# Kernel tuning notes

Measured on AMD Instinct MI355X. Metric: run time of the kernel, lower is better.

The kernel has to match this reference:

```python
import jax, jax.numpy as jnp
import numpy as np

H = 256; NH = 4; DH = H // NH
NT, NS, NV = 4096, 2048, 1024
E1, E2, E3 = 65536, 16384, 32768
LN_EPS = 1e-5


def setup_inputs() -> dict:
    key = jax.random.key(0)
    ks = jax.random.split(key, 40)
    def nrm(i, shape):
        return jax.random.normal(ks[i], shape, jnp.float32) * 0.05
    inp = {
        "x_term": jax.random.normal(ks[0], (NT, H), jnp.float32),
        "x_symbol": jax.random.normal(ks[1], (NS, H), jnp.float32),
        "x_var": jax.random.normal(ks[2], (NV, H), jnp.float32),
        "ha_src": jax.random.randint(ks[3], (E1,), 0, NT),
        "ha_dst": jax.random.randint(ks[4], (E1,), 0, NT),
        "so_src": jax.random.randint(ks[5], (E2,), 0, NT),
        "so_dst": jax.random.randint(ks[6], (E2,), 0, NS),
        "vo_src": jax.random.randint(ks[7], (E3,), 0, NV),
        "vo_dst": jax.random.randint(ks[8], (E3,), 0, NT),
        # SAGEConv params for the 4 term-destination relations
        "Wl_rha": nrm(9, (H, H)),  "bl_rha": nrm(10, (H,)), "Wr_rha": nrm(11, (H, H)),
        "Wl_ha":  nrm(12, (H, H)), "bl_ha":  nrm(13, (H,)), "Wr_ha":  nrm(14, (H, H)),
        "Wl_rsym": nrm(15, (H, H)), "bl_rsym": nrm(16, (H,)), "Wr_rsym": nrm(17, (H, H)),
        "Wl_var": nrm(18, (H, H)), "bl_var": nrm(19, (H,)), "Wr_var": nrm(20, (H, H)),
        "ln_g": jnp.ones((H,), jnp.float32),
        "ln_b": jnp.zeros((H,), jnp.float32),
        "in_proj_w": nrm(21, (3 * H, H)),
        "in_proj_b": nrm(22, (3 * H,)),
        "out_proj_w": nrm(23, (H, H)),
        "out_proj_b": nrm(24, (H,)),
        "post_w": nrm(25, (H, H)),
        "post_b": nrm(26, (H,)),
    }
    return inp


def _sage(x_src, x_dst, src, dst, Wl, bl, Wr, num_dst):
    # PyG SAGEConv: lin_l(mean_j x_src[j]) + lin_r(x_dst)
    msg = x_src[src]                                            # [E, H] gather
    s = jax.ops.segment_sum(msg, dst, num_segments=num_dst)     # [N_dst, H] scatter-add
    cnt = jax.ops.segment_sum(jnp.ones((src.shape[0],), x_src.dtype), dst,
                              num_segments=num_dst)
    agg = s / jnp.maximum(cnt, 1.0)[:, None]
    return agg @ Wl.T + bl + x_dst @ Wr.T


def _layernorm(x, g, b):
    mu = jnp.mean(x, axis=-1, keepdims=True)
    var = jnp.mean(jnp.square(x - mu), axis=-1, keepdims=True)
    return (x - mu) * jax.lax.rsqrt(var + LN_EPS) * g + b


def _mha(x, in_w, in_b, out_w, out_b):
    # torch MultiheadAttention (eval, batch=1, self-attention)
    qkv = x @ in_w.T + in_b                       # [N, 3H]
    q, k, v = jnp.split(qkv, 3, axis=-1)
    def heads(t):
        return t.reshape(-1, NH, DH).transpose(1, 0, 2)  # [NH, N, DH]
    q, k, v = heads(q), heads(k), heads(v)
    scores = jnp.einsum("hqd,hkd->hqk", q, k) / np.sqrt(DH).astype(np.float32)
    a = jax.nn.softmax(scores, axis=-1)
    o = jnp.einsum("hqk,hkd->hqd", a, v)          # [NH, N, DH]
    o = o.transpose(1, 0, 2).reshape(-1, H)
    return o @ out_w.T + out_b


def reference(x_term, x_symbol, x_var,
              ha_src, ha_dst, so_src, so_dst, vo_src, vo_dst,
              Wl_rha, bl_rha, Wr_rha, Wl_ha, bl_ha, Wr_ha,
              Wl_rsym, bl_rsym, Wr_rsym, Wl_var, bl_var, Wr_var,
              ln_g, ln_b, in_proj_w, in_proj_b, out_proj_w, out_proj_b,
              post_w, post_b):
    nt = x_term.shape[0]
    # HeteroConv(aggr='sum') over the 4 relations whose destination is 'term'
    conv_term = (
        _sage(x_term, x_term, ha_dst, ha_src, Wl_rha, bl_rha, Wr_rha, nt)    # rev_has_arg
        + _sage(x_term, x_term, ha_src, ha_dst, Wl_ha, bl_ha, Wr_ha, nt)     # has_arg
        + _sage(x_symbol, x_term, so_dst, so_src, Wl_rsym, bl_rsym, Wr_rsym, nt)  # rev_symbol_of
        + _sage(x_var, x_term, vo_src, vo_dst, Wl_var, bl_var, Wr_var, nt)   # var_occurrence
    )
    term_out = _layernorm(conv_term + x_term, ln_g, ln_b)  # dropout is identity in eval
    attn_out = _mha(term_out, in_proj_w, in_proj_b, out_proj_w, out_proj_b)
    post = jax.nn.relu(attn_out @ post_w.T + post_b)
    term_final = post + term_out
    return term_final
```

## Files before the change

### kernel.cpp

```cpp
#include <hip/hip_runtime.h>
#include <hip/hip_bf16.h>

#define H 256
#define NT 4096
#define NHEAD 4
#define E1 65536
#define E2 16384
#define E3 32768
#define TOTE (2 * E1 + E2 + E3)
#define LN_EPS 1e-5f
#define SPLIT 4

typedef __hip_bfloat16 bf16;
typedef short bf16x8 __attribute__((ext_vector_type(8)));
typedef float f32x4 __attribute__((ext_vector_type(4)));

__device__ __forceinline__ float b2f(bf16 v) { return __bfloat162float(v); }
__device__ __forceinline__ float u2f(unsigned short u) {
    unsigned int x = ((unsigned int)u) << 16;
    return __uint_as_float(x);
}
__device__ __forceinline__ unsigned short f2u(float f) {
    bf16 h = __float2bfloat16(f);
    unsigned short v;
    __builtin_memcpy(&v, &h, 2);
    return v;
}
__device__ __forceinline__ float ldin(const void* p, size_t i, bool isbf) {
    return isbf ? b2f(((const bf16*)p)[i]) : ((const float*)p)[i];
}

__global__ __launch_bounds__(256) void k_init(float4* cnt4, int n4,
                                              const unsigned int* __restrict__ lng,
                                              unsigned int* __restrict__ flag) {
    int i = blockIdx.x * 256 + threadIdx.x;
    if (i == 0) *flag = (lng[0] == 0x3F803F80u) ? 1u : 0u;
    int stride = gridDim.x * 256;
    float4 z = make_float4(0.f, 0.f, 0.f, 0.f);
    for (; i < n4; i += stride) cnt4[i] = z;
}

__global__ __launch_bounds__(256) void k_count4(const int* __restrict__ s0, const int* __restrict__ s1,
                                                const int* __restrict__ s2, const int* __restrict__ s3,
                                                int* __restrict__ cnt) {
    int i = blockIdx.x * 256 + threadIdx.x;
    int r, e;
    if (i < E1) { r = 0; e = i; }
    else if (i < 2 * E1) { r = 1; e = i - E1; }
    else if (i < 2 * E1 + E2) { r = 2; e = i - 2 * E1; }
    else if (i < TOTE) { r = 3; e = i - 2 * E1 - E2; }
    else return;
    const int* s = (r == 0) ? s0 : (r == 1) ? s1 : (r == 2) ? s2 : s3;
    atomicAdd(&cnt[r * NT + s[e]], 1);
}

__global__ __launch_bounds__(256) void k_scan(const int* __restrict__ cnt, int* __restrict__ offs,
                                              int* __restrict__ cursor) {
    __shared__ int tot[256];
    int t = threadIdx.x, r = blockIdx.x;
    const int* c = cnt + r * NT;
    int* o = offs + r * (NT + 1);
    int* cur = cursor + r * NT;
    int base = t * 16;
    int local[16];
    int sum = 0;
#pragma unroll
    for (int j = 0; j < 16; j++) { local[j] = c[base + j]; sum += local[j]; }
    tot[t] = sum;
    __syncthreads();
    if (t == 0) {
        int run = 0;
        for (int i = 0; i < 256; i++) { int v = tot[i]; tot[i] = run; run += v; }
        o[NT] = run;
    }
    __syncthreads();
    int run = tot[t];
#pragma unroll
    for (int j = 0; j < 16; j++) { o[base + j] = run; cur[base + j] = run; run += local[j]; }
}

__global__ __launch_bounds__(256) void k_fill(const int* __restrict__ s0, const int* __restrict__ s1,
                                              const int* __restrict__ s2, const int* __restrict__ s3,
                                              const int* __restrict__ g0, const int* __restrict__ g1,
                                              const int* __restrict__ g2, const int* __restrict__ g3,
                                              int* __restrict__ cursor, int* __restrict__ csr) {
    int i = blockIdx.x * 256 + threadIdx.x;
    int r, e, rb;
    if (i < E1) { r = 0; e = i; rb = 0; }
    else if (i < 2 * E1) { r = 1; e = i - E1; rb = E1; }
    else if (i < 2 * E1 + E2) { r = 2; e = i - 2 * E1; rb = 2 * E1; }
    else if (i < TOTE) { r = 3; e = i - 2 * E1 - E2; rb = 2 * E1 + E2; }
    else return;
    const int* s = (r == 0) ? s0 : (r == 1) ? s1 : (r == 2) ? s2 : s3;
    const int* g = (r == 0) ? g0 : (r == 1) ? g1 : (r == 2) ? g2 : g3;
    int d = s[e];
    int pos = atomicAdd(&cursor[r * NT + d], 1);
    csr[rb + pos] = g[e];
}

__global__ __launch_bounds__(256) void k_gatherA(
    const void* __restrict__ x0, const void* __restrict__ x1,
    const void* __restrict__ x2, const void* __restrict__ x3,
    const int* __restrict__ offs, const int* __restrict__ csr,
    bf16* __restrict__ aggs, const unsigned int* __restrict__ flag) {
    int y = blockIdx.y;
    int i = blockIdx.x * 4 + (threadIdx.x >> 6);
    int lane = threadIdx.x & 63;
    bool isbf = (*flag != 0u);
    const void* x = (y == 0) ? x0 : (y == 1) ? x1 : (y == 2) ? x2 : x3;
    static const int rbase[4] = {0, E1, 2 * E1, 2 * E1 + E2};
    const int* o = offs + y * (NT + 1);
    const int* cs = csr + rbase[y];
    int b = o[i], e = o[i + 1];
    float ax = 0.f, ay = 0.f, az = 0.f, aw = 0.f;
    if (isbf) {
        for (int j = b; j < e; j++) {
            int s = cs[j];
            ushort4 u = *(const ushort4*)((const unsigned short*)x + (size_t)s * H + lane * 4);
            ax += u2f(u.x); ay += u2f(u.y); az += u2f(u.z); aw += u2f(u.w);
        }
    } else {
        for (int j = b; j < e; j++) {
            int s = cs[j];
            float4 v = *(const float4*)((const float*)x + (size_t)s * H + lane * 4);
            ax += v.x; ay += v.y; az += v.z; aw += v.w;
        }
    }
    float inv = 1.0f / fmaxf((float)(e - b), 1.0f);
    *(ushort4*)((unsigned short*)aggs + ((size_t)y * NT + i) * H + lane * 4) =
        make_ushort4(f2u(ax * inv), f2u(ay * inv), f2u(az * inv), f2u(aw * inv));
}

__global__ __launch_bounds__(256) void k_prepB(
    const void* __restrict__ Wl0, const void* __restrict__ Wl1,
    const void* __restrict__ Wl2, const void* __restrict__ Wl3,
    const void* __restrict__ Wr0, const void* __restrict__ Wr1,
    const void* __restrict__ Wr2, const void* __restrict__ Wr3,
    const void* __restrict__ b0, const void* __restrict__ b1,
    const void* __restrict__ b2, const void* __restrict__ b3,
    bf16* __restrict__ Bcat, float* __restrict__ bsum, const unsigned int* __restrict__ flag) {
    int idx = blockIdx.x * 256 + threadIdx.x;
    bool isbf = (*flag != 0u);
    int n = idx / 1280, k = idx % 1280;
    float v;
    if (k < 1024) {
        const void* W = (k < 256) ? Wl0 : (k < 512) ? Wl1 : (k < 768) ? Wl2 : Wl3;
        v = ldin(W, (size_t)n * 256 + (k & 255), isbf);
    } else {
        size_t o = (size_t)n * 256 + (k - 1024);
        v = ldin(Wr0, o, isbf) + ldin(Wr1, o, isbf) + ldin(Wr2, o, isbf) + ldin(Wr3, o, isbf);
    }
    ((unsigned short*)Bcat)[idx] = f2u(v);
    if (idx < 256)
        bsum[idx] = ldin(b0, idx, isbf) + ldin(b1, idx, isbf) + ldin(b2, idx, isbf) + ldin(b3, idx, isbf);
}

__global__ __launch_bounds__(256) void k_convln(
    const bf16* __restrict__ aggs, const bf16* __restrict__ Bcat, const float* __restrict__ bsum,
    const void* __restrict__ xt, const void* __restrict__ gw, const void* __restrict__ gb,
    bf16* __restrict__ term, const unsigned int* __restrict__ flag) {
    __shared__ unsigned short Asm[8 * 16 * 8];
    __shared__ unsigned short Bsm[8 * 256 * 8];
    __shared__ float redS[4][16];
    const bool isbf = (*flag != 0u);
    const int tid = threadIdx.x;
    const int w = tid >> 6, lane = tid & 63;
    const int col = lane & 15, quad = lane >> 4;
    const int m0 = blockIdx.x * 16;
    const int srow = tid & 63, skq = tid >> 6;

    f32x4 acc[4];
#pragma unroll
    for (int dt = 0; dt < 4; dt++) acc[dt] = (f32x4){0.f, 0.f, 0.f, 0.f};

    bf16x8 areg;
    bf16x8 breg[8];
    auto loadA = [&](int k0) {
        if (tid < 128) {
            int row = tid & 15, akq = tid >> 4;
            int k = k0 + akq * 8;
            if (k < 1024) {
                areg = *(const bf16x8*)((const unsigned short*)aggs +
                                        ((size_t)(k >> 8) * NT + m0 + row) * 256 + (k & 255));
            } else {
#pragma unroll
                for (int j = 0; j < 8; j++)
                    areg[j] = (short)f2u(ldin(xt, (size_t)(m0 + row) * 256 + (k - 1024) + j, isbf));
            }
        }
    };
    auto loadB = [&](int k0) {
#pragma unroll
        for (int t = 0; t < 4; t++)
#pragma unroll
            for (int kk = 0; kk < 2; kk++)
                breg[t * 2 + kk] = *(const bf16x8*)((const unsigned short*)Bcat +
                                       (size_t)(t * 64 + srow) * 1280 + k0 + (skq * 2 + kk) * 8);
    };

    loadA(0);
    loadB(0);
    for (int k0 = 0; k0 < 1280; k0 += 64) {
        __syncthreads();
        if (tid < 128) *(bf16x8*)&Asm[tid * 8] = areg;
#pragma unroll
        for (int t = 0; t < 4; t++)
#pragma unroll
            for (int kk = 0; kk < 2; kk++)
                *(bf16x8*)&Bsm[((skq * 2 + kk) * 256 + t * 64 + srow) * 8] = breg[t * 2 + kk];
        __syncthreads();
        if (k0 + 64 < 1280) { loadA(k0 + 64); loadB(k0 + 64); }
#pragma unroll
        for (int ch = 0; ch < 2; ch++) {
            bf16x8 a = *(const bf16x8*)&Asm[(((ch * 4 + quad) & 7) * 16 + col) * 8];
#pragma unroll
            for (int dt = 0; dt < 4; dt++) {
                bf16x8 b = *(const bf16x8*)&Bsm[((ch * 4 + quad) * 256 + w * 64 + dt * 16 + col) * 8];
                acc[dt] = __builtin_amdgcn_mfma_f32_16x16x32_bf16(a, b, acc[dt], 0, 0, 0);
            }
        }
    }

#pragma unroll
    for (int dt = 0; dt < 4; dt++) {
        int n = w * 64 + dt * 16 + col;
        float bsv = bsum[n];
#pragma unroll
        for (int r = 0; r < 4; r++) {
            int m = m0 + quad * 4 + r;
            acc[dt][r] += bsv + ldin(xt, (size_t)m * 256 + n, isbf);
        }
    }
    float mu[4], rs_[4];
#pragma unroll
    for (int r = 0; r < 4; r++) {
        float s = acc[0][r] + acc[1][r] + acc[2][r] + acc[3][r];
#pragma unroll
        for (int mk = 1; mk <= 8; mk <<= 1) s += __shfl_xor(s, mk);
        if (col == 0) redS[w][quad * 4 + r] = s;
    }
    __syncthreads();
#pragma unroll
    for (int r = 0; r < 4; r++) {
        int m = quad * 4 + r;
        mu[r] = (redS[0][m] + redS[1][m] + redS[2][m] + redS[3][m]) * (1.0f / 256.0f);
    }
    __syncthreads();
#pragma unroll
    for (int r = 0; r < 4; r++) {
        float s2 = 0.f;
#pragma unroll
        for (int dt = 0; dt < 4; dt++) {
            float d = acc[dt][r] - mu[r];
            s2 += d * d;
        }
#pragma unroll
        for (int mk = 1; mk <= 8; mk <<= 1) s2 += __shfl_xor(s2, mk);
        if (col == 0) redS[w][quad * 4 + r] = s2;
    }
    __syncthreads();
#pragma unroll
    for (int r = 0; r < 4; r++) {
        int m = quad * 4 + r;
        float var = (redS[0][m] + redS[1][m] + redS[2][m] + redS[3][m]) * (1.0f / 256.0f);
        rs_[r] = rsqrtf(var + LN_EPS);
    }
#pragma unroll
    for (int dt = 0; dt < 4; dt++) {
        int n = w * 64 + dt * 16 + col;
        float gv = ldin(gw, n, isbf), bv = ldin(gb, n, isbf);
#pragma unroll
        for (int r = 0; r < 4; r++) {
            int m = m0 + quad * 4 + r;
            term[(size_t)m * 256 + n] = __float2bfloat16((acc[dt][r] - mu[r]) * rs_[r] * gv + bv);
        }
    }
}

template <int AMODE, int EPI>
__global__ __launch_bounds__(256) void k_gemm(
    const void* __restrict__ A, const void* __restrict__ A2, const float* __restrict__ ml,
    const void* __restrict__ B, const void* __restrict__ bias,
    const bf16* __restrict__ resid, bf16* __restrict__ vt, void* __restrict__ outp,
    int M, int N, int K, const unsigned int* __restrict__ flag) {
    __shared__ unsigned short Asm[4 * 64 * 8];
    __shared__ unsigned short Bsm[4 * 64 * 8];
    const bool isbf = (*flag != 0u);
    const int tid = threadIdx.x;
    const int w = tid >> 6, lane = tid & 63;
    const int col = lane & 15, quad = lane >> 4;
    const int m0 = blockIdx.x * 64, n0 = blockIdx.y * 64;
    const int srow = tid & 63, skq = tid >> 6;
    const int am = m0 + srow;

    f32x4 acc[4];
#pragma unroll
    for (int dt = 0; dt < 4; dt++) acc[dt] = (f32x4){0.f, 0.f, 0.f, 0.f};

    bf16x8 areg, breg;
    auto loadA = [&](int k0) {
        int k = k0 + skq * 8;
        if (AMODE == 0) {
            areg = *(const bf16x8*)((const unsigned short*)A + (size_t)am * K + k);
        } else {
            int h = k >> 6;
            float l0 = ml[(size_t)(0 * NHEAD + h) * NT + am];
            float l1 = ml[(size_t)(1 * NHEAD + h) * NT + am];
            float l2 = ml[(size_t)(2 * NHEAD + h) * NT + am];
            float l3 = ml[(size_t)(3 * NHEAD + h) * NT + am];
            float iw = 1.0f / (l0 + l1 + l2 + l3);
            bf16x8 o0 = *(const bf16x8*)((const unsigned short*)A + (size_t)am * H + k);
            bf16x8 o1 = *(const bf16x8*)((const unsigned short*)A + ((size_t)NT + am) * H + k);
            bf16x8 o2 = *(const bf16x8*)((const unsigned short*)A2 + (size_t)am * H + k);
            bf16x8 o3 = *(const bf16x8*)((const unsigned short*)A2 + ((size_t)NT + am) * H + k);
#pragma unroll
            for (int j = 0; j < 8; j++)
                areg[j] = (short)f2u((l0 * u2f((unsigned short)o0[j]) + l1 * u2f((unsigned short)o1[j]) +
                                      l2 * u2f((unsigned short)o2[j]) + l3 * u2f((unsigned short)o3[j])) * iw);
        }
    };
    auto loadB = [&](int k0) {
        size_t bi = (size_t)(n0 + srow) * K + k0 + skq * 8;
        if (isbf) {
            breg = *(const bf16x8*)((const unsigned short*)B + bi);
        } else {
#pragma unroll
            for (int j = 0; j < 8; j++) breg[j] = (short)f2u(((const float*)B)[bi + j]);
        }
    };

    loadA(0);
    loadB(0);
    for (int k0 = 0; k0 < K; k0 += 32) {
        __syncthreads();
        *(bf16x8*)&Asm[tid * 8] = areg;
        *(bf16x8*)&Bsm[tid * 8] = breg;
        __syncthreads();
        if (k0 + 32 < K) { loadA(k0 + 32); loadB(k0 + 32); }
        bf16x8 a = *(const bf16x8*)&Asm[(quad * 64 + w * 16 + col) * 8];
#pragma unroll
        for (int dt = 0; dt < 4; dt++) {
            bf16x8 b = *(const bf16x8*)&Bsm[(quad * 64 + dt * 16 + col) * 8];
            acc[dt] = __builtin_amdgcn_mfma_f32_16x16x32_bf16(a, b, acc[dt], 0, 0, 0);
        }
    }
#pragma unroll
    for (int dt = 0; dt < 4; dt++) {
        int n = n0 + dt * 16 + col;
        float bv = ldin(bias, n, isbf);
        if (EPI == 3 && n0 >= 512) {
            int m = m0 + w * 16 + quad * 4;
            *(ushort4*)((unsigned short*)vt + (size_t)(n - 512) * NT + m) =
                make_ushort4(f2u(acc[dt][0] + bv), f2u(acc[dt][1] + bv),
                             f2u(acc[dt][2] + bv), f2u(acc[dt][3] + bv));
            continue;
        }
#pragma unroll
        for (int r = 0; r < 4; r++) {
            int m = m0 + w * 16 + quad * 4 + r;
            float v = acc[dt][r] + bv;
            if (EPI == 3) {
                ((bf16*)outp)[(size_t)m * 512 + n] = __float2bfloat16(v);
            } else if (EPI == 2) {
                size_t off = (size_t)m * N + n;
                v = fmaxf(v, 0.f);
                v += b2f(resid[off]);
                ((float*)outp)[off] = v;
            } else {
                ((bf16*)outp)[(size_t)m * N + n] = __float2bfloat16(v);
            }
        }
    }
}

__global__ __launch_bounds__(256) void k_attn(const bf16* __restrict__ qkvQK,
                                              const bf16* __restrict__ vt,
                                              bf16* __restrict__ opart01,
                                              bf16* __restrict__ opart23,
                                              float* __restrict__ ml) {
    __shared__ unsigned short Ksm[8 * 64 * 8];
    __shared__ unsigned short Vsm[8 * 64 * 8];
    __shared__ unsigned short Psm[4][1024];
    const int h = blockIdx.y, sp = blockIdx.z;
    const int q0 = blockIdx.x * 64;
    const int tid = threadIdx.x;
    const int w = tid >> 6, lane = tid & 63;
    const int col = lane & 15, quad = lane >> 4;
    const unsigned short* qk = (const unsigned short*)qkvQK;
    const unsigned short* vp = (const unsigned short*)vt;

    bf16x8 aQ[2];
#pragma unroll
    for (int ch = 0; ch < 2; ch++)
        aQ[ch] = *(const bf16x8*)(qk + (size_t)(q0 + w * 16 + col) * 512 + h * 64 + ch * 32 + quad * 8);

    f32x4 O[4];
#pragma unroll
    for (int dt = 0; dt < 4; dt++) O[dt] = (f32x4){0.f, 0.f, 0.f, 0.f};
    float lsum[4] = {0.f, 0.f, 0.f, 0.f};

    const int kbeg = sp * (NT / SPLIT), kend = kbeg + NT / SPLIT;
    const float SC = 0.125f * 1.44269504f;

    bf16x8 kreg[2], vreg[2];
    auto loadKV = [&](int kb) {
#pragma unroll
        for (int it = 0; it < 2; it++) {
            int cid = tid + it * 256;
            int kkey = cid & 63, dhq = cid >> 6;
            kreg[it] = *(const bf16x8*)(qk + (size_t)(kb + kkey) * 512 + 256 + h * 64 + dhq * 8);
            int vd = cid & 63, vo = cid >> 6;
            vreg[it] = *(const bf16x8*)(vp + (size_t)(h * 64 + vd) * NT + kb + vo * 8);
        }
    };
    loadKV(kbeg);

    for (int kb = kbeg; kb < kend; kb += 64) {
        __syncthreads();
#pragma unroll
        for (int it = 0; it < 2; it++) {
            int cid = tid + it * 256;
            *(bf16x8*)&Ksm[cid * 8] = kreg[it];
            *(bf16x8*)&Vsm[cid * 8] = vreg[it];
        }
        __syncthreads();
        if (kb + 64 < kend) loadKV(kb + 64);

        f32x4 c[4];
#pragma unroll
        for (int dt = 0; dt < 4; dt++) {
            c[dt] = (f32x4){0.f, 0.f, 0.f, 0.f};
#pragma unroll
            for (int ch = 0; ch < 2; ch++) {
                bf16x8 b = *(const bf16x8*)&Ksm[((ch * 4 + quad) * 64 + dt * 16 + col) * 8];
                c[dt] = __builtin_amdgcn_mfma_f32_16x16x32_bf16(aQ[ch], b, c[dt], 0, 0, 0);
            }
#pragma unroll
            for (int r = 0; r < 4; r++) {
                float p = exp2f(c[dt][r] * SC);
                c[dt][r] = p;
                lsum[r] += p;
            }
        }
#pragma unroll
        for (int dt = 0; dt < 4; dt++) {
            int k = dt * 16 + col;
#pragma unroll
            for (int r = 0; r < 4; r++) {
                int ql = quad * 4 + r;
                Psm[w][(k >> 3) * 128 + ql * 8 + (k & 7)] = f2u(c[dt][r]);
            }
        }
        bf16x8 aP[2];
#pragma unroll
        for (int kc = 0; kc < 2; kc++)
            aP[kc] = *(const bf16x8*)&Psm[w][(kc * 4 + quad) * 128 + col * 8];
#pragma unroll
        for (int dt = 0; dt < 4; dt++)
#pragma unroll
            for (int kc = 0; kc < 2; kc++) {
                bf16x8 b = *(const bf16x8*)&Vsm[((kc * 4 + quad) * 64 + dt * 16 + col) * 8];
                O[dt] = __builtin_amdgcn_mfma_f32_16x16x32_bf16(aP[kc], b, O[dt], 0, 0, 0);
            }
    }
    float l[4];
#pragma unroll
    for (int r = 0; r < 4; r++) {
        float s = lsum[r];
#pragma unroll
        for (int mk = 1; mk <= 8; mk <<= 1) s += __shfl_xor(s, mk);
        l[r] = s;
    }
    bf16* ob = (sp < 2) ? (opart01 + (size_t)sp * NT * H) : (opart23 + (size_t)(sp - 2) * NT * H);
#pragma unroll
    for (int dt = 0; dt < 4; dt++) {
#pragma unroll
        for (int r = 0; r < 4; r++) {
            int q = q0 + w * 16 + quad * 4 + r;
            ob[(size_t)q * H + h * 64 + dt * 16 + col] = __float2bfloat16(O[dt][r] / l[r]);
        }
    }
    if (col == 0) {
#pragma unroll
        for (int r = 0; r < 4; r++) {
            int q = q0 + w * 16 + quad * 4 + r;
            ml[((size_t)sp * NHEAD + h) * NT + q] = l[r];
        }
    }
}

extern "C" void kernel_launch(void* const* d_in, const int* in_sizes, int n_in,
                              void* d_out, int out_size, void* d_ws, size_t ws_size,
                              hipStream_t stream) {
    const void* x_term   = d_in[0];
    const void* x_symbol = d_in[1];
    const void* x_var    = d_in[2];
    const int* ha_src = (const int*)d_in[3];
    const int* ha_dst = (const int*)d_in[4];
    const int* so_src = (const int*)d_in[5];
    const int* so_dst = (const int*)d_in[6];
    const int* vo_src = (const int*)d_in[7];
    const int* vo_dst = (const int*)d_in[8];
    const void* Wl[4]  = {d_in[9],  d_in[12], d_in[15], d_in[18]};
    const void* blv[4] = {d_in[10], d_in[13], d_in[16], d_in[19]};
    const void* Wr[4]  = {d_in[11], d_in[14], d_in[17], d_in[20]};
    const void* ln_g = d_in[21];
    const void* ln_b = d_in[22];
    const void* in_w = d_in[23];
    const void* in_b = d_in[24];
    const void* out_w = d_in[25];
    const void* out_b = d_in[26];
    const void* post_w = d_in[27];
    const void* post_b = d_in[28];

    char* ws = (char*)d_ws;
    unsigned int* flag = (unsigned int*)ws;
    char* csrbase = ws + 256;
    int* cnt    = (int*)csrbase;
    int* offs   = (int*)(csrbase + 65536);
    int* cursor = (int*)(csrbase + 132096);
    int* csr    = (int*)(csrbase + 197632);
    bf16*  Bcat = (bf16*)csrbase;
    float* bsum = (float*)(csrbase + 655360);
    float* ml   = (float*)csrbase;
    bf16* aggs  = (bf16*)(ws + (1 << 20));
    bf16* term  = (bf16*)(ws + (1 << 20) + 8388608);
    bf16* opart23 = (bf16*)(ws + (1 << 20) + 10485760);
    bf16* qkvQK = aggs;
    bf16* vt    = (bf16*)((char*)aggs + 4194304);
    bf16* proj  = aggs;
    bf16* opart01 = (bf16*)d_out;

    k_init<<<16, 256, 0, stream>>>((float4*)cnt, 4 * NT / 4, (const unsigned int*)ln_g, flag);
    k_count4<<<(TOTE + 255) / 256, 256, 0, stream>>>(ha_src, ha_dst, so_src, vo_dst, cnt);
    k_scan<<<4, 256, 0, stream>>>(cnt, offs, cursor);
    k_fill<<<(TOTE + 255) / 256, 256, 0, stream>>>(ha_src, ha_dst, so_src, vo_dst,
                                                   ha_dst, ha_src, so_dst, vo_src, cursor, csr);
    k_gatherA<<<dim3(NT / 4, 4), 256, 0, stream>>>(x_term, x_term, x_symbol, x_var,
                                                   offs, csr, aggs, flag);
    k_prepB<<<(256 * 1280) / 256, 256, 0, stream>>>(Wl[0], Wl[1], Wl[2], Wl[3],
                                                    Wr[0], Wr[1], Wr[2], Wr[3],
                                                    blv[0], blv[1], blv[2], blv[3],
                                                    Bcat, bsum, flag);

    k_convln<<<256, 256, 0, stream>>>(aggs, Bcat, bsum, x_term, ln_g, ln_b, term, flag);

    k_gemm<0, 3><<<dim3(64, 12), 256, 0, stream>>>(
        term, nullptr, nullptr, in_w, in_b, nullptr, vt, qkvQK, NT, 768, 256, flag);

    k_attn<<<dim3(64, NHEAD, SPLIT), 256, 0, stream>>>(qkvQK, vt, opart01, opart23, ml);

    k_gemm<1, 0><<<dim3(64, 4), 256, 0, stream>>>(
        opart01, opart23, ml, out_w, out_b, nullptr, nullptr, proj, NT, 256, 256, flag);

    k_gemm<0, 2><<<dim3(64, 4), 256, 0, stream>>>(
        proj, nullptr, nullptr, post_w, post_b, term, nullptr, d_out, NT, 256, 256, flag);

    (void)in_sizes; (void)n_in; (void)out_size; (void)ws_size;
}
```

Baseline: 283.4 us.

## Process two query tiles per attention block to reuse K/V tiles

Each attention block now handles 128 queries (two 64-query tiles per wave set) instead of 64, so every K/V tile staged in shared memory feeds twice as many MFMAs. The grid is halved along the query axis. P is also packed to bf16 by truncation instead of round-to-nearest, which saves conversion instructions but adds a slight bias. Register pressure and LDS use go up, and with only 512 blocks occupancy may drop.

```diff
diff --git a/kernel.cpp b/kernel.cpp
--- a/kernel.cpp
+++ b/kernel.cpp
@@ -25,6 +25,9 @@
     unsigned short v;
     __builtin_memcpy(&v, &h, 2);
     return v;
+}
+__device__ __forceinline__ unsigned short f2u_rtz(float f) {
+    return (unsigned short)(__float_as_uint(f) >> 16);
 }
 __device__ __forceinline__ float ldin(const void* p, size_t i, bool isbf) {
     return isbf ? b2f(((const bf16*)p)[i]) : ((const float*)p)[i];
@@ -380,24 +383,29 @@
                                               float* __restrict__ ml) {
     __shared__ unsigned short Ksm[8 * 64 * 8];
     __shared__ unsigned short Vsm[8 * 64 * 8];
-    __shared__ unsigned short Psm[4][1024];
+    __shared__ unsigned short Psm[4][2048];
     const int h = blockIdx.y, sp = blockIdx.z;
-    const int q0 = blockIdx.x * 64;
+    const int q0 = blockIdx.x * 128;
     const int tid = threadIdx.x;
     const int w = tid >> 6, lane = tid & 63;
     const int col = lane & 15, quad = lane >> 4;
     const unsigned short* qk = (const unsigned short*)qkvQK;
     const unsigned short* vp = (const unsigned short*)vt;
 
-    bf16x8 aQ[2];
-#pragma unroll
-    for (int ch = 0; ch < 2; ch++)
-        aQ[ch] = *(const bf16x8*)(qk + (size_t)(q0 + w * 16 + col) * 512 + h * 64 + ch * 32 + quad * 8);
-
-    f32x4 O[4];
-#pragma unroll
-    for (int dt = 0; dt < 4; dt++) O[dt] = (f32x4){0.f, 0.f, 0.f, 0.f};
-    float lsum[4] = {0.f, 0.f, 0.f, 0.f};
+    bf16x8 aQ[2][2];
+#pragma unroll
+    for (int qt = 0; qt < 2; qt++)
+#pragma unroll
+        for (int ch = 0; ch < 2; ch++)
+            aQ[qt][ch] = *(const bf16x8*)(qk + (size_t)(q0 + qt * 64 + w * 16 + col) * 512 +
+                                          h * 64 + ch * 32 + quad * 8);
+
+    f32x4 O[2][4];
+#pragma unroll
+    for (int qt = 0; qt < 2; qt++)
+#pragma unroll
+        for (int dt = 0; dt < 4; dt++) O[qt][dt] = (f32x4){0.f, 0.f, 0.f, 0.f};
+    float lsum[2][4] = {};
 
     const int kbeg = sp * (NT / SPLIT), kend = kbeg + NT / SPLIT;
     const float SC = 0.125f * 1.44269504f;
@@ -426,65 +434,71 @@
         __syncthreads();
         if (kb + 64 < kend) loadKV(kb + 64);
 
-        f32x4 c[4];
+        f32x4 c0[4], c1[4];
 #pragma unroll
         for (int dt = 0; dt < 4; dt++) {
-            c[dt] = (f32x4){0.f, 0.f, 0.f, 0.f};
+            c0[dt] = (f32x4){0.f, 0.f, 0.f, 0.f};
+            c1[dt] = (f32x4){0.f, 0.f, 0.f, 0.f};
 #pragma unroll
             for (int ch = 0; ch < 2; ch++) {
                 bf16x8 b = *(const bf16x8*)&Ksm[((ch * 4 + quad) * 64 + dt * 16 + col) * 8];
-                c[dt] = __builtin_amdgcn_mfma_f32_16x16x32_bf16(aQ[ch], b, c[dt], 0, 0, 0);
-            }
-#pragma unroll
-            for (int r = 0; r < 4; r++) {
-                float p = exp2f(c[dt][r] * SC);
-                c[dt][r] = p;
-                lsum[r] += p;
-            }
-        }
-#pragma unroll
-        for (int dt = 0; dt < 4; dt++) {
-            int k = dt * 16 + col;
-#pragma unroll
-            for (int r = 0; r < 4; r++) {
-                int ql = quad * 4 + r;
-                Psm[w][(k >> 3) * 128 + ql * 8 + (k & 7)] = f2u(c[dt][r]);
-            }
-        }
-        bf16x8 aP[2];
-#pragma unroll
-        for (int kc = 0; kc < 2; kc++)
-            aP[kc] = *(const bf16x8*)&Psm[w][(kc * 4 + quad) * 128 + col * 8];
+                c0[dt] = __builtin_amdgcn_mfma_f32_16x16x32_bf16(aQ[0][ch], b, c0[dt], 0, 0, 0);
+                c1[dt] = __builtin_amdgcn_mfma_f32_16x16x32_bf16(aQ[1][ch], b, c1[dt], 0, 0, 0);
+            }
+        }
+#pragma unroll
+        for (int qt = 0; qt < 2; qt++) {
+#pragma unroll
+            for (int dt = 0; dt < 4; dt++) {
+                int k = dt * 16 + col;
+#pragma unroll
+                for (int r = 0; r < 4; r++) {
+                    float p = exp2f((qt ? c1[dt][r] : c0[dt][r]) * SC);
+                    lsum[qt][r] += p;
+                    Psm[w][qt * 1024 + (k >> 3) * 128 + (quad * 4 + r) * 8 + (k & 7)] = f2u_rtz(p);
+                }
+            }
+        }
+        bf16x8 aP[2][2];
+#pragma unroll
+        for (int qt = 0; qt < 2; qt++)
+#pragma unroll
+            for (int kc = 0; kc < 2; kc++)
+                aP[qt][kc] = *(const bf16x8*)&Psm[w][qt * 1024 + (kc * 4 + quad) * 128 + col * 8];
 #pragma unroll
         for (int dt = 0; dt < 4; dt++)
 #pragma unroll
             for (int kc = 0; kc < 2; kc++) {
                 bf16x8 b = *(const bf16x8*)&Vsm[((kc * 4 + quad) * 64 + dt * 16 + col) * 8];
-                O[dt] = __builtin_amdgcn_mfma_f32_16x16x32_bf16(aP[kc], b, O[dt], 0, 0, 0);
-            }
-    }
-    float l[4];
-#pragma unroll
-    for (int r = 0; r < 4; r++) {
-        float s = lsum[r];
-#pragma unroll
-        for (int mk = 1; mk <= 8; mk <<= 1) s += __shfl_xor(s, mk);
-        l[r] = s;
-    }
-    bf16* ob = (sp < 2) ? (opart01 + (size_t)sp * NT * H) : (opart23 + (size_t)(sp - 2) * NT * H);
-#pragma unroll
-    for (int dt = 0; dt < 4; dt++) {
+                O[0][dt] = __builtin_amdgcn_mfma_f32_16x16x32_bf16(aP[0][kc], b, O[0][dt], 0, 0, 0);
+                O[1][dt] = __builtin_amdgcn_mfma_f32_16x16x32_bf16(aP[1][kc], b, O[1][dt], 0, 0, 0);
+            }
+    }
+#pragma unroll
+    for (int qt = 0; qt < 2; qt++) {
+        float l[4];
 #pragma unroll
         for (int r = 0; r < 4; r++) {
-            int q = q0 + w * 16 + quad * 4 + r;
-            ob[(size_t)q * H + h * 64 + dt * 16 + col] = __float2bfloat16(O[dt][r] / l[r]);
-        }
-    }
-    if (col == 0) {
-#pragma unroll
-        for (int r = 0; r < 4; r++) {
-            int q = q0 + w * 16 + quad * 4 + r;
-            ml[((size_t)sp * NHEAD + h) * NT + q] = l[r];
+            float s = lsum[qt][r];
+#pragma unroll
+            for (int mk = 1; mk <= 8; mk <<= 1) s += __shfl_xor(s, mk);
+            l[r] = s;
+        }
+        bf16* ob = (sp < 2) ? (opart01 + (size_t)sp * NT * H) : (opart23 + (size_t)(sp - 2) * NT * H);
+#pragma unroll
+        for (int dt = 0; dt < 4; dt++) {
+#pragma unroll
+            for (int r = 0; r < 4; r++) {
+                int q = q0 + qt * 64 + w * 16 + quad * 4 + r;
+                ob[(size_t)q * H + h * 64 + dt * 16 + col] = __float2bfloat16(O[qt][dt][r] / l[r]);
+            }
+        }
+        if (col == 0) {
+#pragma unroll
+            for (int r = 0; r < 4; r++) {
+                int q = q0 + qt * 64 + w * 16 + quad * 4 + r;
+                ml[((size_t)sp * NHEAD + h) * NT + q] = l[r];
+            }
         }
     }
 }
@@ -548,7 +562,7 @@
     k_gemm<0, 3><<<dim3(64, 12), 256, 0, stream>>>(
         term, nullptr, nullptr, in_w, in_b, nullptr, vt, qkvQK, NT, 768, 256, flag);
 
-    k_attn<<<dim3(64, NHEAD, SPLIT), 256, 0, stream>>>(qkvQK, vt, opart01, opart23, ml);
+    k_attn<<<dim3(32, NHEAD, SPLIT), 256, 0, stream>>>(qkvQK, vt, opart01, opart23, ml);
 
     k_gemm<1, 0><<<dim3(64, 4), 256, 0, stream>>>(
         opart01, opart23, ml, out_w, out_b, nullptr, nullptr, proj, NT, 256, 256, flag);
```

Measured after the change: 278.7 us. Within noise of the previous version (-1.7%).
